# Kernel tuning notes

Measured on AMD Instinct MI355X. Metric: run time of the kernel, lower is better.

The kernel has to match this reference:

```python
import jax, jax.numpy as jnp
import numpy as np

# Static graph dimensions (mirror mat_wann config)
B, IN_DIM, NH, NO = 16384, 512, 128, 256
DENSITY = 0.03


def _build_adjacency():
    """Build the static sparse connectivity matrix.

    mat is [NH + NO, IN_DIM + NH]; entry values: 0 = no edge, 1 = linear edge
    (weight only), 2/3/4 = weight then tanh/relu/sigmoid. Hidden rows only read
    input columns (hidden->hidden block zero), output rows read inputs+hiddens.
    Edge order (for weight assignment) is row-major, as in the torch module.
    """
    rng = np.random.default_rng(0)
    p = DENSITY
    probs = [1.0 - p, p / 4, p / 4, p / 4, p / 4]
    mat_h = rng.choice(5, size=(NH, IN_DIM), p=probs)            # hidden rows (input cols only)
    mat_o = rng.choice(5, size=(NO, IN_DIM + NH), p=probs)       # output rows
    rows_h, cols_h = np.nonzero(mat_h)
    acts_h = mat_h[rows_h, cols_h]
    rows_o, cols_o = np.nonzero(mat_o)
    acts_o = mat_o[rows_o, cols_o]
    return (rows_h.astype(np.int32), cols_h.astype(np.int32), acts_h.astype(np.int32),
            rows_o.astype(np.int32), cols_o.astype(np.int32), acts_o.astype(np.int32))


def setup_inputs() -> dict:
    rows_h, cols_h, acts_h, rows_o, cols_o, acts_o = _build_adjacency()
    key = jax.random.key(0)
    kx, kh, ko = jax.random.split(key, 3)
    x = jax.random.normal(kx, (B, IN_DIM), dtype=jnp.float32)
    # one learned scalar weight per edge (nn.Linear(1,1,bias=False) each)
    wh = jax.random.normal(kh, (rows_h.shape[0],), dtype=jnp.float32) * 0.5
    wo = jax.random.normal(ko, (rows_o.shape[0],), dtype=jnp.float32) * 0.5
    return {
        "x": x, "wh": wh, "wo": wo,
        "rows_h": jnp.asarray(rows_h), "cols_h": jnp.asarray(cols_h), "acts_h": jnp.asarray(acts_h),
        "rows_o": jnp.asarray(rows_o), "cols_o": jnp.asarray(cols_o), "acts_o": jnp.asarray(acts_o),
    }


def _edge_act(z, acts):
    # act id 1 -> identity (weight only); 2 -> tanh; 3 -> relu; 4 -> sigmoid
    return jnp.where(acts == 2, jnp.tanh(z),
           jnp.where(acts == 3, jax.nn.relu(z),
           jnp.where(acts == 4, jax.nn.sigmoid(z), z)))


def reference(x, wh, wo, rows_h, cols_h, acts_h, rows_o, cols_o, acts_o):
    # hidden nodes: per-edge scalar weight + per-edge activation, scatter-add to dest
    zh = _edge_act(x[:, cols_h] * wh, acts_h)                     # [B, Eh]
    H = jnp.zeros((x.shape[0], NH), x.dtype).at[:, rows_h].add(zh)  # [B, NH]
    src = jnp.concatenate([x, H], axis=1)                         # [B, IN+NH]
    zo = _edge_act(src[:, cols_o] * wo, acts_o)                   # [B, Eo]
    out = jnp.zeros((x.shape[0], NO), x.dtype).at[:, rows_o].add(zo)
    return jnp.tanh(out)                                          # output_activation
```

## Files before the change

kernel.cpp:

```cpp
#include <hip/hip_runtime.h>
#include <math.h>

#define BATCH   16384
#define IN_DIM  512
#define NH      128
#define NO      256
#define L2E     1.4426950408889634f

__device__ __forceinline__ float fast_rcp(float x) { return __builtin_amdgcn_rcpf(x); }
__device__ __forceinline__ float fast_exp2(float x) {
#if __has_builtin(__builtin_amdgcn_exp2f)
    return __builtin_amdgcn_exp2f(x);
#else
    return exp2f(x);
#endif
}
__device__ __forceinline__ int rfl(int v) { return __builtin_amdgcn_readfirstlane(v); }

__device__ __forceinline__ float fast_tanh(float z) {
    float ex = fast_exp2(2.f * L2E * z);
    return 1.f - 2.f * fast_rcp(1.f + ex);
}
__device__ __forceinline__ float fast_sig(float z) {
    float ex = fast_exp2(-L2E * z);
    return fast_rcp(1.f + ex);
}
__device__ __forceinline__ float act_k(int a) {
    return (a == 2) ? (2.f * L2E) : ((a == 4) ? -L2E : 0.f);
}

__device__ __forceinline__ void acc_act4(float4& acc, float4 v, float w, int a) {
    float zx = v.x * w, zy = v.y * w, zz = v.z * w, zw = v.w * w;
    if (a == 2) {
        acc.x += fast_tanh(zx); acc.y += fast_tanh(zy);
        acc.z += fast_tanh(zz); acc.w += fast_tanh(zw);
    } else if (a == 4) {
        acc.x += fast_sig(zx); acc.y += fast_sig(zy);
        acc.z += fast_sig(zz); acc.w += fast_sig(zw);
    } else if (a == 3) {
        acc.x += fmaxf(zx, 0.f); acc.y += fmaxf(zy, 0.f);
        acc.z += fmaxf(zz, 0.f); acc.w += fmaxf(zw, 0.f);
    } else {
        acc.x += zx; acc.y += zy; acc.z += zz; acc.w += zw;
    }
}

__device__ __forceinline__ unsigned int f2bf_rne(float f) {
    unsigned int u = __float_as_uint(f);
    return (u + 0x7FFFu + ((u >> 16) & 1u)) >> 16;
}
__device__ __forceinline__ float bf_lo(unsigned int u) { return __uint_as_float(u << 16); }
__device__ __forceinline__ float bf_hi(unsigned int u) { return __uint_as_float(u & 0xFFFF0000u); }

__device__ __forceinline__ int lower_bound_dev(const int* __restrict__ arr, int n, int v) {
    int lo = 0, hi = n;
    while (lo < hi) { int m = (lo + hi) >> 1; if (arr[m] < v) lo = m + 1; else hi = m; }
    return lo;
}

__device__ __forceinline__ float4 run_hidden_row(const unsigned short* __restrict__ xt,
                                                 const int4* __restrict__ packed_h,
                                                 int e0, int e1, int bi) {
    float4 acc = make_float4(0.f, 0.f, 0.f, 0.f);
    #pragma unroll 4
    for (int e = e0; e < e1; ++e) {
        int4 p  = packed_h[e];
        int col = rfl(p.x);
        int a   = rfl(p.y);
        float w = __int_as_float(rfl(p.z));
        uint2 uu = *(const uint2*)(xt + (size_t)col * BATCH + bi);
        float4 v = make_float4(bf_lo(uu.x), bf_hi(uu.x), bf_lo(uu.y), bf_hi(uu.y));
        acc_act4(acc, v, w, a);
    }
    return acc;
}
__device__ __forceinline__ float4 run_output_row(const unsigned short* __restrict__ xt,
                                                 const float* __restrict__ Ht,
                                                 const int4* __restrict__ packed_o,
                                                 int e0, int e1, int bi) {
    float4 acc = make_float4(0.f, 0.f, 0.f, 0.f);
    #pragma unroll 4
    for (int e = e0; e < e1; ++e) {
        int4 p  = packed_o[e];
        int col = rfl(p.x);
        int a   = rfl(p.y);
        float w = __int_as_float(rfl(p.z));
        float4 v;
        if (col < IN_DIM) {
            uint2 uu = *(const uint2*)(xt + (size_t)col * BATCH + bi);
            v = make_float4(bf_lo(uu.x), bf_hi(uu.x), bf_lo(uu.y), bf_hi(uu.y));
        } else {
            v = *(const float4*)&Ht[(size_t)(col - IN_DIM) * BATCH + bi];
        }
        acc_act4(acc, v, w, a);
    }
    return acc;
}

__device__ __forceinline__ void decode_slice(int bid, int& s, int& rg) {
    int xcd = bid & 7;
    int m   = bid >> 3;
    rg      = m & 15;
    int u   = m >> 4;
    s = ((u >> 1) << 4) | (xcd << 1) | (u & 1);
}

__global__ __launch_bounds__(256)
void prep_fused(const float* __restrict__ x, unsigned short* __restrict__ xt,
                const int* __restrict__ rows_h, const int* __restrict__ cols_h,
                const int* __restrict__ acts_h, const float* __restrict__ wh,
                const int* __restrict__ rows_o, const int* __restrict__ cols_o,
                const int* __restrict__ acts_o, const float* __restrict__ wo,
                int Eh, int Eo, int tile_blocks,
                int* __restrict__ offs_h, int* __restrict__ offs_o,
                int4* __restrict__ packed_h, int4* __restrict__ packed_o) {
    extern __shared__ float tile[];
    if ((int)blockIdx.x < tile_blocks) {
        const int bt = blockIdx.x & (BATCH / 128 - 1);
        const int ct = blockIdx.x >> 7;
        const int b0 = bt * 128, c0 = ct * 128;
        #pragma unroll
        for (int it = 0; it < 16; ++it) {
            int v = threadIdx.x + it * 256;
            int b = v >> 5, i = v & 31;
            float4 f = *(const float4*)&x[(size_t)(b0 + b) * IN_DIM + c0 + i * 4];
            float* d = &tile[b * 129 + i * 4];
            d[0] = f.x; d[1] = f.y; d[2] = f.z; d[3] = f.w;
        }
        __syncthreads();
        #pragma unroll
        for (int it = 0; it < 8; ++it) {
            int v = threadIdx.x + it * 256;
            int c = v >> 4, j = v & 15;
            int b = j * 8;
            unsigned int uu[4];
            #pragma unroll
            for (int q = 0; q < 4; ++q) {
                float lo = tile[(b + 2 * q)     * 129 + c];
                float hi = tile[(b + 2 * q + 1) * 129 + c];
                uu[q] = f2bf_rne(lo) | (f2bf_rne(hi) << 16);
            }
            *(uint4*)&xt[(size_t)(c0 + c) * BATCH + b0 + b] = make_uint4(uu[0], uu[1], uu[2], uu[3]);
        }
        return;
    }
    int t = (blockIdx.x - tile_blocks) * 256 + threadIdx.x;
    if (t <= NH) offs_h[t] = lower_bound_dev(rows_h, Eh, t);
    else if (t <= NH + 1 + NO) offs_o[t - (NH + 1)] = lower_bound_dev(rows_o, Eo, t - (NH + 1));
    int u = t - (NH + 1 + NO + 1);
    if (u >= 0 && u < Eh) {
        int a = acts_h[u];
        packed_h[u] = make_int4(cols_h[u], a, __float_as_int(wh[u]), 0);
    }
    u -= Eh;
    if (u >= 0 && u < Eo) {
        int a = acts_o[u];
        packed_o[u] = make_int4(cols_o[u], a, __float_as_int(wo[u]), 0);
    }
}

__global__ __launch_bounds__(512)
void hidden_kernel(const unsigned short* __restrict__ xt, const int* __restrict__ offs_h,
                   const int4* __restrict__ packed_h, float* __restrict__ Ht) {
    const int lane = threadIdx.x & 63;
    const int wv   = threadIdx.x >> 6;
    int s, rg;
    decode_slice(blockIdx.x, s, rg);
    const int bi = s * 256 + lane * 4;
    const int r  = rg * 8 + wv;
    const int e0 = rfl(offs_h[r]);
    const int e1 = rfl(offs_h[r + 1]);
    float4 acc = run_hidden_row(xt, packed_h, e0, e1, bi);
    *(float4*)&Ht[(size_t)r * BATCH + bi] = acc;
}

#define OBS 260
__global__ __launch_bounds__(512)
void output_kernel(const unsigned short* __restrict__ xt, const float* __restrict__ Ht,
                   const int* __restrict__ offs_o, const int4* __restrict__ packed_o,
                   float* __restrict__ out) {
    __shared__ float OB[16 * OBS];
    const int lane = threadIdx.x & 63;
    const int wv   = threadIdx.x >> 6;
    int s, rg;
    decode_slice(blockIdx.x, s, rg);
    const int rb = s * 256;
    const int r0 = rg * 16;
    const int bi = rb + lane * 4;
    #pragma unroll
    for (int rr = wv * 2; rr < wv * 2 + 2; ++rr) {
        const int r  = r0 + rr;
        const int e0 = rfl(offs_o[r]);
        const int e1 = rfl(offs_o[r + 1]);
        float4 acc = run_output_row(xt, Ht, packed_o, e0, e1, bi);
        OB[rr * OBS + lane * 4 + 0] = fast_tanh(acc.x);
        OB[rr * OBS + lane * 4 + 1] = fast_tanh(acc.y);
        OB[rr * OBS + lane * 4 + 2] = fast_tanh(acc.z);
        OB[rr * OBS + lane * 4 + 3] = fast_tanh(acc.w);
    }
    __syncthreads();
    #pragma unroll
    for (int it = 0; it < 2; ++it) {
        int v  = threadIdx.x + it * 512;
        int c4 = v & 3;
        int b  = v >> 2;
        float4 o;
        o.x = OB[(c4 * 4 + 0) * OBS + b];
        o.y = OB[(c4 * 4 + 1) * OBS + b];
        o.z = OB[(c4 * 4 + 2) * OBS + b];
        o.w = OB[(c4 * 4 + 3) * OBS + b];
        *(float4*)&out[(size_t)(rb + b) * NO + r0 + c4 * 4] = o;
    }
}

#define FT      1024
#define FBPB    64
#define FXS     514
#define FHS     65
#define FOBTS   260
#define FLDS    (99072 + 1544)
__device__ __forceinline__ unsigned short f2bf16s(float f) { return (unsigned short)f2bf_rne(f); }
__device__ __forceinline__ float bf2f(unsigned short h) { return __uint_as_float(((unsigned int)h) << 16); }
__device__ __forceinline__ float edge_act2(float z, int a, float k) {
    float ex = fast_exp2(k * z);
    float rc = fast_rcp(1.f + ex);
    return (a == 2) ? (1.f - 2.f * rc) : ((a == 4) ? rc : ((a == 3) ? fmaxf(z, 0.f) : z));
}
__global__ __launch_bounds__(FT)
void wann_fused(const float* __restrict__ x,
                const int* __restrict__ rows_h, const int* __restrict__ cols_h,
                const int* __restrict__ acts_h, const float* __restrict__ wh,
                const int* __restrict__ rows_o, const int* __restrict__ cols_o,
                const int* __restrict__ acts_o, const float* __restrict__ wo,
                float* __restrict__ out, int Eh, int Eo)
{
    extern __shared__ char lds[];
    unsigned short* X   = (unsigned short*)lds;
    float*          H   = (float*)(lds + 65792);
    float*          OBT = (float*)lds;
    int*            offsH = (int*)(lds + 99072);
    int*            offsO = offsH + (NH + 1);
    const int tid  = threadIdx.x;
    const int lane = tid & 63;
    const int wv   = tid >> 6;
    const int rb   = blockIdx.x * FBPB;
    const int* wh_i = (const int*)wh;
    const int* wo_i = (const int*)wo;
    {
        const float4* xv = (const float4*)(x + (size_t)rb * IN_DIM);
        #pragma unroll
        for (int kk = 0; kk < (FBPB * IN_DIM / 4) / FT; ++kk) {
            int v = tid + kk * FT;
            int r = v >> 7, i = v & 127;
            float4 f = xv[v];
            unsigned int lo = (unsigned int)f2bf16s(f.x) | ((unsigned int)f2bf16s(f.y) << 16);
            unsigned int hi = (unsigned int)f2bf16s(f.z) | ((unsigned int)f2bf16s(f.w) << 16);
            unsigned int* dst = (unsigned int*)&X[r * FXS + i * 4];
            dst[0] = lo; dst[1] = hi;
        }
    }
    if (tid <= NH) offsH[tid] = lower_bound_dev(rows_h, Eh, tid);
    else if (tid <= NH + 1 + NO) offsO[tid - (NH + 1)] = lower_bound_dev(rows_o, Eo, tid - (NH + 1));
    __syncthreads();
    for (int r = wv * (NH / 16); r < (wv + 1) * (NH / 16); ++r) {
        const int e0 = rfl(offsH[r]); const int e1 = rfl(offsH[r + 1]);
        float acc = 0.f;
        #pragma unroll 4
        for (int e = e0; e < e1; ++e) {
            int col = rfl(cols_h[e]); int a = rfl(acts_h[e]);
            float w = __int_as_float(rfl(wh_i[e]));
            acc += edge_act2(bf2f(X[lane * FXS + col]) * w, a, act_k(a));
        }
        H[r * FHS + lane] = acc;
    }
    __syncthreads();
    float res[NO / 16];
    #pragma unroll
    for (int rr = 0; rr < NO / 16; ++rr) {
        const int r = wv * (NO / 16) + rr;
        const int e0 = rfl(offsO[r]); const int e1 = rfl(offsO[r + 1]);
        float acc = 0.f;
        #pragma unroll 4
        for (int e = e0; e < e1; ++e) {
            int col = rfl(cols_o[e]); int a = rfl(acts_o[e]);
            float w = __int_as_float(rfl(wo_i[e]));
            float v = (col < IN_DIM) ? bf2f(X[lane * FXS + col]) : H[(col - IN_DIM) * FHS + lane];
            acc += edge_act2(v * w, a, act_k(a));
        }
        res[rr] = fast_tanh(acc);
    }
    __syncthreads();
    #pragma unroll
    for (int rr = 0; rr < NO / 16; ++rr)
        OBT[lane * FOBTS + wv * (NO / 16) + rr] = res[rr];
    __syncthreads();
    #pragma unroll
    for (int kk = 0; kk < (FBPB * NO / 4) / FT; ++kk) {
        int v = tid + kk * FT;
        int c4 = v & 63, b = v >> 6;
        float4 o = *(const float4*)&OBT[b * FOBTS + c4 * 4];
        *(float4*)&out[(size_t)(rb + b) * NO + c4 * 4] = o;
    }
}

extern "C" void kernel_launch(void* const* d_in, const int* in_sizes, int n_in,
                              void* d_out, int out_size, void* d_ws, size_t ws_size,
                              hipStream_t stream) {
    const float* x      = (const float*)d_in[0];
    const float* wh     = (const float*)d_in[1];
    const float* wo     = (const float*)d_in[2];
    const int*   rows_h = (const int*)d_in[3];
    const int*   cols_h = (const int*)d_in[4];
    const int*   acts_h = (const int*)d_in[5];
    const int*   rows_o = (const int*)d_in[6];
    const int*   cols_o = (const int*)d_in[7];
    const int*   acts_o = (const int*)d_in[8];
    float*       out    = (float*)d_out;

    const int Eh = in_sizes[1];
    const int Eo = in_sizes[2];

    char* ws = (char*)d_ws;
    int*  offs_h   = (int*)ws;
    int*  offs_o   = (int*)(ws + 1024);
    int4* packed_h = (int4*)(ws + 4096);
    int4* packed_o = packed_h + Eh;
    size_t tier_packed = 4096 + (size_t)(Eh + Eo) * 16;
    size_t xt_off      = (tier_packed + 255) & ~(size_t)255;
    unsigned short* xt = (unsigned short*)(ws + xt_off);
    size_t ht_off      = (xt_off + (size_t)IN_DIM * BATCH * 2 + 255) & ~(size_t)255;
    float* Ht          = (float*)(ws + ht_off);
    size_t need_full   = ht_off + (size_t)NH * BATCH * 4;

    if (ws_size >= need_full) {
        const int ntasks      = (NH + 1) + (NO + 1) + Eh + Eo;
        const int edge_blocks = (ntasks + 255) / 256;
        const int tile_blocks = (BATCH / 128) * (IN_DIM / 128);
        prep_fused<<<tile_blocks + edge_blocks, 256, 128 * 129 * 4, stream>>>(
            x, xt, rows_h, cols_h, acts_h, wh, rows_o, cols_o, acts_o, wo,
            Eh, Eo, tile_blocks, offs_h, offs_o, packed_h, packed_o);
        hidden_kernel<<<1024, 512, 0, stream>>>(xt, offs_h, packed_h, Ht);
        output_kernel<<<1024, 512, 0, stream>>>(xt, Ht, offs_o, packed_o, out);
    } else {
        wann_fused<<<BATCH / FBPB, FT, FLDS, stream>>>(
            x, rows_h, cols_h, acts_h, wh, rows_o, cols_o, acts_o, wo, out, Eh, Eo);
    }
}
```

Measured before the change: 141.7 us.

## Fuse hidden and output stages into one LDS-resident per-batch-tile kernel

Replaces the three-kernel pipeline (global transpose of x to bf16, hidden kernel writing Ht to global, output kernel) with a small edge-packing kernel plus one fused kernel. Each 1024-thread block loads 64 batch rows of x into LDS as bf16, computes hidden nodes into LDS, then output nodes, and writes the result through an LDS transpose. This removes the global round-trips of the transposed x and Ht and two launches. In exchange each thread handles a single batch element instead of four, LDS use is large (about 99 KB per block), and the gathered LDS reads may hit bank conflicts.

```diff
diff --git a/kernel.cpp b/kernel.cpp
--- a/kernel.cpp
+++ b/kernel.cpp
@@ -29,28 +29,19 @@
     return (a == 2) ? (2.f * L2E) : ((a == 4) ? -L2E : 0.f);
 }
 
-__device__ __forceinline__ void acc_act4(float4& acc, float4 v, float w, int a) {
-    float zx = v.x * w, zy = v.y * w, zz = v.z * w, zw = v.w * w;
-    if (a == 2) {
-        acc.x += fast_tanh(zx); acc.y += fast_tanh(zy);
-        acc.z += fast_tanh(zz); acc.w += fast_tanh(zw);
-    } else if (a == 4) {
-        acc.x += fast_sig(zx); acc.y += fast_sig(zy);
-        acc.z += fast_sig(zz); acc.w += fast_sig(zw);
-    } else if (a == 3) {
-        acc.x += fmaxf(zx, 0.f); acc.y += fmaxf(zy, 0.f);
-        acc.z += fmaxf(zz, 0.f); acc.w += fmaxf(zw, 0.f);
-    } else {
-        acc.x += zx; acc.y += zy; acc.z += zz; acc.w += zw;
-    }
+__device__ __forceinline__ float act1(float z, int a) {
+    if (a == 2) return fast_tanh(z);
+    if (a == 4) return fast_sig(z);
+    if (a == 3) return fmaxf(z, 0.f);
+    return z;
 }
 
 __device__ __forceinline__ unsigned int f2bf_rne(float f) {
     unsigned int u = __float_as_uint(f);
     return (u + 0x7FFFu + ((u >> 16) & 1u)) >> 16;
 }
-__device__ __forceinline__ float bf_lo(unsigned int u) { return __uint_as_float(u << 16); }
-__device__ __forceinline__ float bf_hi(unsigned int u) { return __uint_as_float(u & 0xFFFF0000u); }
+__device__ __forceinline__ float bf2f(unsigned short h) { return __uint_as_float(((unsigned int)h) << 16); }
+__device__ __forceinline__ unsigned short f2bf16s(float f) { return (unsigned short)f2bf_rne(f); }
 
 __device__ __forceinline__ int lower_bound_dev(const int* __restrict__ arr, int n, int v) {
     int lo = 0, hi = n;
@@ -58,169 +49,117 @@
     return lo;
 }
 
-__device__ __forceinline__ float4 run_hidden_row(const unsigned short* __restrict__ xt,
-                                                 const int4* __restrict__ packed_h,
-                                                 int e0, int e1, int bi) {
-    float4 acc = make_float4(0.f, 0.f, 0.f, 0.f);
-    #pragma unroll 4
-    for (int e = e0; e < e1; ++e) {
-        int4 p  = packed_h[e];
-        int col = rfl(p.x);
-        int a   = rfl(p.y);
-        float w = __int_as_float(rfl(p.z));
-        uint2 uu = *(const uint2*)(xt + (size_t)col * BATCH + bi);
-        float4 v = make_float4(bf_lo(uu.x), bf_hi(uu.x), bf_lo(uu.y), bf_hi(uu.y));
-        acc_act4(acc, v, w, a);
-    }
-    return acc;
-}
-__device__ __forceinline__ float4 run_output_row(const unsigned short* __restrict__ xt,
-                                                 const float* __restrict__ Ht,
-                                                 const int4* __restrict__ packed_o,
-                                                 int e0, int e1, int bi) {
-    float4 acc = make_float4(0.f, 0.f, 0.f, 0.f);
-    #pragma unroll 4
-    for (int e = e0; e < e1; ++e) {
-        int4 p  = packed_o[e];
-        int col = rfl(p.x);
-        int a   = rfl(p.y);
-        float w = __int_as_float(rfl(p.z));
-        float4 v;
-        if (col < IN_DIM) {
-            uint2 uu = *(const uint2*)(xt + (size_t)col * BATCH + bi);
-            v = make_float4(bf_lo(uu.x), bf_hi(uu.x), bf_lo(uu.y), bf_hi(uu.y));
-        } else {
-            v = *(const float4*)&Ht[(size_t)(col - IN_DIM) * BATCH + bi];
-        }
-        acc_act4(acc, v, w, a);
-    }
-    return acc;
-}
-
-__device__ __forceinline__ void decode_slice(int bid, int& s, int& rg) {
-    int xcd = bid & 7;
-    int m   = bid >> 3;
-    rg      = m & 15;
-    int u   = m >> 4;
-    s = ((u >> 1) << 4) | (xcd << 1) | (u & 1);
-}
-
 __global__ __launch_bounds__(256)
-void prep_fused(const float* __restrict__ x, unsigned short* __restrict__ xt,
-                const int* __restrict__ rows_h, const int* __restrict__ cols_h,
+void prep_edges(const int* __restrict__ rows_h, const int* __restrict__ cols_h,
                 const int* __restrict__ acts_h, const float* __restrict__ wh,
                 const int* __restrict__ rows_o, const int* __restrict__ cols_o,
                 const int* __restrict__ acts_o, const float* __restrict__ wo,
-                int Eh, int Eo, int tile_blocks,
+                int Eh, int Eo,
                 int* __restrict__ offs_h, int* __restrict__ offs_o,
                 int4* __restrict__ packed_h, int4* __restrict__ packed_o) {
-    extern __shared__ float tile[];
-    if ((int)blockIdx.x < tile_blocks) {
-        const int bt = blockIdx.x & (BATCH / 128 - 1);
-        const int ct = blockIdx.x >> 7;
-        const int b0 = bt * 128, c0 = ct * 128;
-        #pragma unroll
-        for (int it = 0; it < 16; ++it) {
-            int v = threadIdx.x + it * 256;
-            int b = v >> 5, i = v & 31;
-            float4 f = *(const float4*)&x[(size_t)(b0 + b) * IN_DIM + c0 + i * 4];
-            float* d = &tile[b * 129 + i * 4];
-            d[0] = f.x; d[1] = f.y; d[2] = f.z; d[3] = f.w;
-        }
-        __syncthreads();
-        #pragma unroll
-        for (int it = 0; it < 8; ++it) {
-            int v = threadIdx.x + it * 256;
-            int c = v >> 4, j = v & 15;
-            int b = j * 8;
-            unsigned int uu[4];
-            #pragma unroll
-            for (int q = 0; q < 4; ++q) {
-                float lo = tile[(b + 2 * q)     * 129 + c];
-                float hi = tile[(b + 2 * q + 1) * 129 + c];
-                uu[q] = f2bf_rne(lo) | (f2bf_rne(hi) << 16);
-            }
-            *(uint4*)&xt[(size_t)(c0 + c) * BATCH + b0 + b] = make_uint4(uu[0], uu[1], uu[2], uu[3]);
-        }
-        return;
-    }
-    int t = (blockIdx.x - tile_blocks) * 256 + threadIdx.x;
+    int t = blockIdx.x * 256 + threadIdx.x;
     if (t <= NH) offs_h[t] = lower_bound_dev(rows_h, Eh, t);
     else if (t <= NH + 1 + NO) offs_o[t - (NH + 1)] = lower_bound_dev(rows_o, Eo, t - (NH + 1));
     int u = t - (NH + 1 + NO + 1);
-    if (u >= 0 && u < Eh) {
-        int a = acts_h[u];
-        packed_h[u] = make_int4(cols_h[u], a, __float_as_int(wh[u]), 0);
-    }
+    if (u >= 0 && u < Eh)
+        packed_h[u] = make_int4(cols_h[u], acts_h[u], __float_as_int(wh[u]), 0);
     u -= Eh;
-    if (u >= 0 && u < Eo) {
-        int a = acts_o[u];
-        packed_o[u] = make_int4(cols_o[u], a, __float_as_int(wo[u]), 0);
-    }
-}
-
-__global__ __launch_bounds__(512)
-void hidden_kernel(const unsigned short* __restrict__ xt, const int* __restrict__ offs_h,
-                   const int4* __restrict__ packed_h, float* __restrict__ Ht) {
-    const int lane = threadIdx.x & 63;
-    const int wv   = threadIdx.x >> 6;
-    int s, rg;
-    decode_slice(blockIdx.x, s, rg);
-    const int bi = s * 256 + lane * 4;
-    const int r  = rg * 8 + wv;
-    const int e0 = rfl(offs_h[r]);
-    const int e1 = rfl(offs_h[r + 1]);
-    float4 acc = run_hidden_row(xt, packed_h, e0, e1, bi);
-    *(float4*)&Ht[(size_t)r * BATCH + bi] = acc;
-}
-
-#define OBS 260
-__global__ __launch_bounds__(512)
-void output_kernel(const unsigned short* __restrict__ xt, const float* __restrict__ Ht,
-                   const int* __restrict__ offs_o, const int4* __restrict__ packed_o,
-                   float* __restrict__ out) {
-    __shared__ float OB[16 * OBS];
-    const int lane = threadIdx.x & 63;
-    const int wv   = threadIdx.x >> 6;
-    int s, rg;
-    decode_slice(blockIdx.x, s, rg);
-    const int rb = s * 256;
-    const int r0 = rg * 16;
-    const int bi = rb + lane * 4;
-    #pragma unroll
-    for (int rr = wv * 2; rr < wv * 2 + 2; ++rr) {
-        const int r  = r0 + rr;
+    if (u >= 0 && u < Eo)
+        packed_o[u] = make_int4(cols_o[u], acts_o[u], __float_as_int(wo[u]), 0);
+}
+
+#define FXS   514
+#define FHS   65
+#define FOBS  260
+#define FLDSZ 99072
+__global__ __launch_bounds__(1024)
+void fused_main(const float* __restrict__ x,
+                const int* __restrict__ offs_h, const int4* __restrict__ packed_h,
+                const int* __restrict__ offs_o, const int4* __restrict__ packed_o,
+                float* __restrict__ out)
+{
+    extern __shared__ char lds[];
+    unsigned short* X   = (unsigned short*)lds;
+    float*          H   = (float*)(lds + 65792);
+    float*          OBT = (float*)lds;
+    const int tid  = threadIdx.x;
+    const int lane = tid & 63;
+    const int wv   = tid >> 6;
+    const int rb   = blockIdx.x * 64;
+
+    {
+        const float4* xv = (const float4*)(x + (size_t)rb * IN_DIM);
+        #pragma unroll
+        for (int kk = 0; kk < 8; ++kk) {
+            int v = tid + kk * 1024;
+            int r = v >> 7, i = v & 127;
+            float4 f = xv[v];
+            unsigned int lo = f2bf_rne(f.x) | (f2bf_rne(f.y) << 16);
+            unsigned int hi = f2bf_rne(f.z) | (f2bf_rne(f.w) << 16);
+            unsigned int* dst = (unsigned int*)&X[r * FXS + i * 4];
+            dst[0] = lo; dst[1] = hi;
+        }
+    }
+    __syncthreads();
+
+    #pragma unroll
+    for (int rr = 0; rr < NH / 16; ++rr) {
+        const int r  = wv * (NH / 16) + rr;
+        const int e0 = rfl(offs_h[r]);
+        const int e1 = rfl(offs_h[r + 1]);
+        float acc = 0.f;
+        #pragma unroll 4
+        for (int e = e0; e < e1; ++e) {
+            int4 p  = packed_h[e];
+            int col = rfl(p.x);
+            int a   = rfl(p.y);
+            float w = __int_as_float(rfl(p.z));
+            acc += act1(bf2f(X[lane * FXS + col]) * w, a);
+        }
+        H[r * FHS + lane] = acc;
+    }
+    __syncthreads();
+
+    float res[NO / 16];
+    #pragma unroll
+    for (int rr = 0; rr < NO / 16; ++rr) {
+        const int r  = wv * (NO / 16) + rr;
         const int e0 = rfl(offs_o[r]);
         const int e1 = rfl(offs_o[r + 1]);
-        float4 acc = run_output_row(xt, Ht, packed_o, e0, e1, bi);
-        OB[rr * OBS + lane * 4 + 0] = fast_tanh(acc.x);
-        OB[rr * OBS + lane * 4 + 1] = fast_tanh(acc.y);
-        OB[rr * OBS + lane * 4 + 2] = fast_tanh(acc.z);
-        OB[rr * OBS + lane * 4 + 3] = fast_tanh(acc.w);
-    }
-    __syncthreads();
-    #pragma unroll
-    for (int it = 0; it < 2; ++it) {
-        int v  = threadIdx.x + it * 512;
-        int c4 = v & 3;
-        int b  = v >> 2;
-        float4 o;
-        o.x = OB[(c4 * 4 + 0) * OBS + b];
-        o.y = OB[(c4 * 4 + 1) * OBS + b];
-        o.z = OB[(c4 * 4 + 2) * OBS + b];
-        o.w = OB[(c4 * 4 + 3) * OBS + b];
-        *(float4*)&out[(size_t)(rb + b) * NO + r0 + c4 * 4] = o;
+        float acc = 0.f;
+        #pragma unroll 4
+        for (int e = e0; e < e1; ++e) {
+            int4 p  = packed_o[e];
+            int col = rfl(p.x);
+            int a   = rfl(p.y);
+            float w = __int_as_float(rfl(p.z));
+            float v = (col < IN_DIM) ? bf2f(X[lane * FXS + col])
+                                     : H[(col - IN_DIM) * FHS + lane];
+            acc += act1(v * w, a);
+        }
+        res[rr] = fast_tanh(acc);
+    }
+    __syncthreads();
+
+    #pragma unroll
+    for (int rr = 0; rr < NO / 16; ++rr)
+        OBT[lane * FOBS + wv * (NO / 16) + rr] = res[rr];
+    __syncthreads();
+    #pragma unroll
+    for (int kk = 0; kk < 4; ++kk) {
+        int v  = tid + kk * 1024;
+        int c4 = v & 63;
+        int b  = v >> 6;
+        float4 o = *(const float4*)&OBT[b * FOBS + c4 * 4];
+        *(float4*)&out[(size_t)(rb + b) * NO + c4 * 4] = o;
     }
 }
 
 #define FT      1024
 #define FBPB    64
-#define FXS     514
-#define FHS     65
+#define FHS2    65
 #define FOBTS   260
 #define FLDS    (99072 + 1544)
-__device__ __forceinline__ unsigned short f2bf16s(float f) { return (unsigned short)f2bf_rne(f); }
-__device__ __forceinline__ float bf2f(unsigned short h) { return __uint_as_float(((unsigned int)h) << 16); }
 __device__ __forceinline__ float edge_act2(float z, int a, float k) {
     float ex = fast_exp2(k * z);
     float rc = fast_rcp(1.f + ex);
@@ -271,7 +210,7 @@
             float w = __int_as_float(rfl(wh_i[e]));
             acc += edge_act2(bf2f(X[lane * FXS + col]) * w, a, act_k(a));
         }
-        H[r * FHS + lane] = acc;
+        H[r * FHS2 + lane] = acc;
     }
     __syncthreads();
     float res[NO / 16];
@@ -284,7 +223,7 @@
         for (int e = e0; e < e1; ++e) {
             int col = rfl(cols_o[e]); int a = rfl(acts_o[e]);
             float w = __int_as_float(rfl(wo_i[e]));
-            float v = (col < IN_DIM) ? bf2f(X[lane * FXS + col]) : H[(col - IN_DIM) * FHS + lane];
+            float v = (col < IN_DIM) ? bf2f(X[lane * FXS + col]) : H[(col - IN_DIM) * FHS2 + lane];
             acc += edge_act2(v * w, a, act_k(a));
         }
         res[rr] = fast_tanh(acc);
@@ -325,22 +264,15 @@
     int*  offs_o   = (int*)(ws + 1024);
     int4* packed_h = (int4*)(ws + 4096);
     int4* packed_o = packed_h + Eh;
-    size_t tier_packed = 4096 + (size_t)(Eh + Eo) * 16;
-    size_t xt_off      = (tier_packed + 255) & ~(size_t)255;
-    unsigned short* xt = (unsigned short*)(ws + xt_off);
-    size_t ht_off      = (xt_off + (size_t)IN_DIM * BATCH * 2 + 255) & ~(size_t)255;
-    float* Ht          = (float*)(ws + ht_off);
-    size_t need_full   = ht_off + (size_t)NH * BATCH * 4;
-
-    if (ws_size >= need_full) {
-        const int ntasks      = (NH + 1) + (NO + 1) + Eh + Eo;
-        const int edge_blocks = (ntasks + 255) / 256;
-        const int tile_blocks = (BATCH / 128) * (IN_DIM / 128);
-        prep_fused<<<tile_blocks + edge_blocks, 256, 128 * 129 * 4, stream>>>(
-            x, xt, rows_h, cols_h, acts_h, wh, rows_o, cols_o, acts_o, wo,
-            Eh, Eo, tile_blocks, offs_h, offs_o, packed_h, packed_o);
-        hidden_kernel<<<1024, 512, 0, stream>>>(xt, offs_h, packed_h, Ht);
-        output_kernel<<<1024, 512, 0, stream>>>(xt, Ht, offs_o, packed_o, out);
+    size_t need = 4096 + (size_t)(Eh + Eo) * 16;
+
+    if (ws_size >= need) {
+        const int ntasks = (NH + 1) + (NO + 1) + Eh + Eo;
+        prep_edges<<<(ntasks + 255) / 256, 256, 0, stream>>>(
+            rows_h, cols_h, acts_h, wh, rows_o, cols_o, acts_o, wo,
+            Eh, Eo, offs_h, offs_o, packed_h, packed_o);
+        fused_main<<<BATCH / 64, 1024, FLDSZ, stream>>>(
+            x, offs_h, packed_h, offs_o, packed_o, out);
     } else {
         wann_fused<<<BATCH / FBPB, FT, FLDS, stream>>>(
             x, rows_h, cols_h, acts_h, wh, rows_o, cols_o, acts_o, wo, out, Eh, Eo);
```

After: 191.1 us. 34.9% more time.
